# Kernel optimization log

Measured on AMD Instinct MI355X. Metric: run time of the kernel, lower is better.

## Reference

```python
import jax, jax.numpy as jnp
import numpy as np
import math

HEAD = 4
HEAD_DIM = 16
K_ATT = 7
PAD_ATT = 3  # (dilation*(kernel_att-1)+1)//2 with dilation=1, kernel_att=7
K_CONV = 3


def closest_factor_to_sqrt(n):
    if n <= 1:
        return n
    sqrt_n = int(math.sqrt(n))
    if sqrt_n * sqrt_n == n:
        return sqrt_n
    best, best_diff = 1, float('inf')
    for i in range(sqrt_n, 0, -1):
        if n % i == 0:
            diff = abs(i - n // i)
            if diff < best_diff:
                best_diff, best = diff, i
    return best


def setup_inputs() -> dict:
    key = jax.random.key(0)
    ks = jax.random.split(key, 10)
    Cin, Cout = 64, 64
    x = jax.random.normal(ks[0], (2, Cin, 8, 32, 32), dtype=jnp.float32)
    w1 = jax.random.normal(ks[1], (Cout, Cin), dtype=jnp.float32) * 0.05
    b1 = jax.random.normal(ks[2], (Cout,), dtype=jnp.float32) * 0.01
    w2 = jax.random.normal(ks[3], (Cout, Cin), dtype=jnp.float32) * 0.05
    b2 = jax.random.normal(ks[4], (Cout,), dtype=jnp.float32) * 0.01
    w3 = jax.random.normal(ks[5], (Cout, Cin), dtype=jnp.float32) * 0.05
    b3 = jax.random.normal(ks[6], (Cout,), dtype=jnp.float32) * 0.01
    wp = jax.random.normal(ks[7], (HEAD_DIM, 3), dtype=jnp.float32) * 0.05
    bp = jnp.zeros((HEAD_DIM,), dtype=jnp.float32)
    wfc = jax.random.normal(ks[8], (K_CONV * K_CONV, 3 * HEAD), dtype=jnp.float32) * 0.05
    # dep_conv init per reset_parameters(): identity shift kernels, zero bias
    ident = jnp.eye(K_CONV * K_CONV, dtype=jnp.float32).reshape(K_CONV * K_CONV, K_CONV, K_CONV)
    wdep = jnp.tile(ident[None], (Cout, 1, 1, 1))  # (Cout, 9, 3, 3), groups=head_dim
    bdep = jnp.zeros((Cout,), dtype=jnp.float32)
    rate1 = jnp.array(0.5, dtype=jnp.float32)
    rate2 = jnp.array(0.5, dtype=jnp.float32)
    return {'x': x, 'w1': w1, 'b1': b1, 'w2': w2, 'b2': b2, 'w3': w3, 'b3': b3,
            'wp': wp, 'bp': bp, 'wfc': wfc, 'wdep': wdep, 'bdep': bdep,
            'rate1': rate1, 'rate2': rate2}


def _forward(x, w1, b1, w2, b2, w3, b3, wp, bp, wfc, wdep, bdep, rate1, rate2):
    conv1x1 = lambda t, wm, bias: jnp.einsum('oc,bcdwh->bodwh', wm, t) + bias[None, :, None, None, None]
    q = conv1x1(x, w1, b1)
    k = conv1x1(x, w2, b2)
    v = conv1x1(x, w3, b3)
    b, C, d, w, h = q.shape
    scaling = HEAD_DIM ** -0.5
    fh = closest_factor_to_sqrt(d)
    fw = d // fh
    H2, W2 = fh * h, fw * w  # flat reshape of (d, w, h) -> (H2, W2)

    # position encoding, torch position(d, h, w) -> (1, 3, d, w, h)
    loc_d = jnp.broadcast_to(jnp.linspace(-1.0, 1.0, d)[:, None, None], (d, w, h))
    loc_w = jnp.broadcast_to(jnp.linspace(-1.0, 1.0, w)[None, :, None], (d, w, h))
    loc_h = jnp.broadcast_to(jnp.linspace(-1.0, 1.0, h)[None, None, :], (d, w, h))
    loc = jnp.stack([loc_d, loc_w, loc_h], 0)[None].astype(x.dtype)
    pe = (jnp.einsum('oc,bcdwh->bodwh', wp, loc) + bp[None, :, None, None, None])
    pe = pe.reshape(1, HEAD_DIM, H2, W2)

    q_att = (q * scaling).reshape(b * HEAD, HEAD_DIM, H2, W2)
    k_att = k.reshape(b * HEAD, HEAD_DIM, H2, W2)
    v_att = v.reshape(b * HEAD, HEAD_DIM, H2, W2)

    def unfold(t):
        # nn.Unfold(kernel=7, stride=1) after ReflectionPad2d(3): (N, C, 49, H2, W2)
        p = jnp.pad(t, ((0, 0), (0, 0), (PAD_ATT, PAD_ATT), (PAD_ATT, PAD_ATT)), mode='reflect')
        return jnp.stack([p[:, :, i:i + H2, j:j + W2]
                          for i in range(K_ATT) for j in range(K_ATT)], axis=2)

    unfold_k = unfold(k_att)            # (b*head, hd, 49, H2, W2)
    unfold_rpe = unfold(pe)             # (1, hd, 49, H2, W2)
    scores = unfold_k + pe[:, :, None] - unfold_rpe
    att = jnp.einsum('nchw,nckhw->nkhw', q_att, scores)  # sum over head_dim
    att = jax.nn.softmax(att, axis=1)   # softmax over 49 window positions
    out_att = jnp.einsum('nkhw,nckhw->nchw', att, unfold(v_att))
    out_att = out_att.reshape(b, C, d, w, h)

    # conv-mixing branch
    L = d * w * h
    qkv = jnp.concatenate([q.reshape(b, HEAD, HEAD_DIM, L),
                           k.reshape(b, HEAD, HEAD_DIM, L),
                           v.reshape(b, HEAD, HEAD_DIM, L)], axis=1)  # (b, 3*head, hd, L)
    # fc: 1x1x1 conv over the 3*head channel axis (torch applies it unbatched after permute)
    f_all = jnp.einsum('oc,bcml->boml', wfc, qkv)         # (b, 9, hd, L)
    f_conv = f_all.reshape(b, K_CONV * K_CONV * HEAD_DIM, d, h * w)
    out_conv = jax.lax.conv_general_dilated(
        f_conv, wdep, window_strides=(1, 1), padding=[(1, 1), (1, 1)],
        dimension_numbers=('NCHW', 'OIHW', 'NCHW'), feature_group_count=HEAD_DIM)
    out_conv = out_conv + bdep[None, :, None, None]
    out_conv = out_conv.reshape(b, C, d, w, h)

    return rate1 * out_att + rate2 * out_conv


def reference(x, w1, b1, w2, b2, w3, b3, wp, bp, wfc, wdep, bdep, rate1, rate2):
    return _forward(x, w1, b1, w2, b2, w3, b3, wp, bp, wfc, wdep, bdep, rate1, rate2)
```

## Files before the change

### kernel.cpp

```cpp
#include <hip/hip_runtime.h>


__global__ __launch_bounds__(512) void qkvf_kernel(
    const float* __restrict__ x,
    const float* __restrict__ w1, const float* __restrict__ b1,
    const float* __restrict__ w2, const float* __restrict__ b2,
    const float* __restrict__ w3, const float* __restrict__ b3,
    const float* __restrict__ wfc,
    float* __restrict__ q, float* __restrict__ k, float* __restrict__ v,
    float* __restrict__ f)
{
    __shared__ float xs[64][64];
    __shared__ float wlds[3][64][64];

    int bx    = blockIdx.x;
    int ltile = bx & 127;
    int b     = bx >> 7;
    int l0    = ltile * 64;

    {
        float4* wl = (float4*)wlds;
        for (int t = threadIdx.x; t < 3072; t += 512) {
            int m   = t >> 10;
            int idx = t & 1023;
            const float* src = (m == 0) ? w1 : (m == 1) ? w2 : w3;
            wl[t] = ((const float4*)src)[idx];
        }
    }
    const float4* xg = (const float4*)(x + (size_t)b * 64 * 8192);
    for (int t = threadIdx.x; t < 1024; t += 512) {
        int ci = t >> 4, col = t & 15;
        *((float4*)&xs[ci][col * 4]) = xg[ci * 2048 + (l0 >> 2) + col];
    }
    __syncthreads();

    int lane = threadIdx.x & 63;
    int wv   = __builtin_amdgcn_readfirstlane(threadIdx.x >> 6);
    int l    = l0 + lane;
    int hd0  = 2 * wv;

    float qa[4][2], ka[4][2], va[4][2];
#pragma unroll
    for (int hh = 0; hh < 4; ++hh)
#pragma unroll
        for (int p = 0; p < 2; ++p) {
            int c = hh * 16 + hd0 + p;
            qa[hh][p] = b1[c]; ka[hh][p] = b2[c]; va[hh][p] = b3[c];
        }

#pragma unroll 4
    for (int c4 = 0; c4 < 16; ++c4) {
        float xv[4];
#pragma unroll
        for (int u = 0; u < 4; ++u) xv[u] = xs[c4 * 4 + u][lane];
#pragma unroll
        for (int hh = 0; hh < 4; ++hh)
#pragma unroll
            for (int p = 0; p < 2; ++p) {
                int c = hh * 16 + hd0 + p;
                float4 wq = *(const float4*)&wlds[0][c][c4 * 4];
                float4 wk = *(const float4*)&wlds[1][c][c4 * 4];
                float4 wx = *(const float4*)&wlds[2][c][c4 * 4];
                qa[hh][p] = fmaf(wq.x, xv[0], qa[hh][p]);
                qa[hh][p] = fmaf(wq.y, xv[1], qa[hh][p]);
                qa[hh][p] = fmaf(wq.z, xv[2], qa[hh][p]);
                qa[hh][p] = fmaf(wq.w, xv[3], qa[hh][p]);
                ka[hh][p] = fmaf(wk.x, xv[0], ka[hh][p]);
                ka[hh][p] = fmaf(wk.y, xv[1], ka[hh][p]);
                ka[hh][p] = fmaf(wk.z, xv[2], ka[hh][p]);
                ka[hh][p] = fmaf(wk.w, xv[3], ka[hh][p]);
                va[hh][p] = fmaf(wx.x, xv[0], va[hh][p]);
                va[hh][p] = fmaf(wx.y, xv[1], va[hh][p]);
                va[hh][p] = fmaf(wx.z, xv[2], va[hh][p]);
                va[hh][p] = fmaf(wx.w, xv[3], va[hh][p]);
            }
    }

#pragma unroll
    for (int hh = 0; hh < 4; ++hh)
#pragma unroll
        for (int p = 0; p < 2; ++p) {
            int c = hh * 16 + hd0 + p;
            size_t o = (size_t)(b * 64 + c) * 8192 + l;
            q[o] = qa[hh][p]; k[o] = ka[hh][p]; v[o] = va[hh][p];
        }

#pragma unroll
    for (int m = 0; m < 9; ++m)
#pragma unroll
        for (int p = 0; p < 2; ++p) {
            float acc = 0.f;
#pragma unroll
            for (int hh = 0; hh < 4; ++hh) {
                acc = fmaf(wfc[m * 12 + 0 + hh], qa[hh][p], acc);
                acc = fmaf(wfc[m * 12 + 4 + hh], ka[hh][p], acc);
                acc = fmaf(wfc[m * 12 + 8 + hh], va[hh][p], acc);
            }
            int hd = hd0 + p;
            f[((size_t)(b * 9 + m) * 16 + hd) * 8192 + l] = acc;
        }
}

__global__ __launch_bounds__(256) void att_kernel(
    const float* __restrict__ q, const float* __restrict__ k,
    const float* __restrict__ v,
    const float* __restrict__ wp, const float* __restrict__ bp,
    const float* __restrict__ rate1p, float* __restrict__ out)
{
    __shared__ float kp[22][22][20];
    __shared__ float vt[22][22][20];

    int bx = blockIdx.x;
    int xt = bx & 7;
    int yt = (bx >> 3) & 3;
    int n  = bx >> 5;
    int head = n & 3;
    int b    = n >> 2;
    int y0 = yt * 16, x0 = xt * 16;

    const int NELEM = 16 * 22 * 22;
    for (int e = threadIdx.x; e < NELEM; e += 256) {
        int tx  = e % 22;
        int rem = e / 22;
        int ty  = rem % 22;
        int c   = rem / 22;
        int sy = y0 + ty - 3; if (sy < 0) sy = -sy; else if (sy >= 64)  sy = 126 - sy;
        int sx = x0 + tx - 3; if (sx < 0) sx = -sx; else if (sx >= 128) sx = 254 - sx;
        int l = sy * 128 + sx;
        size_t o = (size_t)(b * 64 + head * 16 + c) * 8192 + l;
        int dd = l >> 10, r2 = l & 1023, ww = r2 >> 5, hh = r2 & 31;
        float ld = dd * (2.0f / 7.0f)  - 1.0f;
        float lw = ww * (2.0f / 31.0f) - 1.0f;
        float lh = hh * (2.0f / 31.0f) - 1.0f;
        float pe = bp[c];
        pe = fmaf(wp[c * 3 + 0], ld, pe);
        pe = fmaf(wp[c * 3 + 1], lw, pe);
        pe = fmaf(wp[c * 3 + 2], lh, pe);
        kp[ty][tx][c] = k[o] - pe;
        vt[ty][tx][c] = v[o];
    }
    __syncthreads();

    int tx = threadIdx.x & 15, ty = threadIdx.x >> 4;
    int l = (y0 + ty) * 128 + (x0 + tx);

    float qc[16];
#pragma unroll
    for (int c = 0; c < 16; ++c)
        qc[c] = q[(size_t)(b * 64 + head * 16 + c) * 8192 + l] * 0.25f;

    float lg[49];
#pragma unroll
    for (int i = 0; i < 7; ++i)
#pragma unroll
        for (int j = 0; j < 7; ++j) {
            const float4* p = (const float4*)&kp[ty + i][tx + j][0];
            float4 a = p[0], b4 = p[1], c4 = p[2], d4 = p[3];
            float acc =      qc[0]  * a.x;
            acc = fmaf(qc[1],  a.y,  acc); acc = fmaf(qc[2],  a.z,  acc);
            acc = fmaf(qc[3],  a.w,  acc); acc = fmaf(qc[4],  b4.x, acc);
            acc = fmaf(qc[5],  b4.y, acc); acc = fmaf(qc[6],  b4.z, acc);
            acc = fmaf(qc[7],  b4.w, acc); acc = fmaf(qc[8],  c4.x, acc);
            acc = fmaf(qc[9],  c4.y, acc); acc = fmaf(qc[10], c4.z, acc);
            acc = fmaf(qc[11], c4.w, acc); acc = fmaf(qc[12], d4.x, acc);
            acc = fmaf(qc[13], d4.y, acc); acc = fmaf(qc[14], d4.z, acc);
            acc = fmaf(qc[15], d4.w, acc);
            lg[i * 7 + j] = acc;
        }

    float mx = lg[0];
#pragma unroll
    for (int kk = 1; kk < 49; ++kk) mx = fmaxf(mx, lg[kk]);
    float se = 0.f;
#pragma unroll
    for (int kk = 0; kk < 49; ++kk) { lg[kk] = __expf(lg[kk] - mx); se += lg[kk]; }
    float scale = rate1p[0] / se;

    float oc[16];
#pragma unroll
    for (int c = 0; c < 16; ++c) oc[c] = 0.f;
#pragma unroll
    for (int i = 0; i < 7; ++i)
#pragma unroll
        for (int j = 0; j < 7; ++j) {
            float wgt = lg[i * 7 + j];
            const float4* p = (const float4*)&vt[ty + i][tx + j][0];
            float4 a = p[0], b4 = p[1], c4 = p[2], d4 = p[3];
            oc[0]  = fmaf(wgt, a.x,  oc[0]);  oc[1]  = fmaf(wgt, a.y,  oc[1]);
            oc[2]  = fmaf(wgt, a.z,  oc[2]);  oc[3]  = fmaf(wgt, a.w,  oc[3]);
            oc[4]  = fmaf(wgt, b4.x, oc[4]);  oc[5]  = fmaf(wgt, b4.y, oc[5]);
            oc[6]  = fmaf(wgt, b4.z, oc[6]);  oc[7]  = fmaf(wgt, b4.w, oc[7]);
            oc[8]  = fmaf(wgt, c4.x, oc[8]);  oc[9]  = fmaf(wgt, c4.y, oc[9]);
            oc[10] = fmaf(wgt, c4.z, oc[10]); oc[11] = fmaf(wgt, c4.w, oc[11]);
            oc[12] = fmaf(wgt, d4.x, oc[12]); oc[13] = fmaf(wgt, d4.y, oc[13]);
            oc[14] = fmaf(wgt, d4.z, oc[14]); oc[15] = fmaf(wgt, d4.w, oc[15]);
        }

#pragma unroll
    for (int c = 0; c < 16; ++c)
        out[(size_t)(b * 64 + head * 16 + c) * 8192 + l] = oc[c] * scale;
}

__global__ __launch_bounds__(256) void conv_kernel(
    const float* __restrict__ f,
    const float* __restrict__ wdep, const float* __restrict__ bdep,
    const float* __restrict__ rate2p, float* __restrict__ out)
{
    __shared__ float ft[9][8][130];

    int bx = blockIdx.x;
    int xt = bx & 7;
    int g  = (bx >> 3) & 15;
    int b  = bx >> 7;
    int x0 = xt * 128;

    const int NE = 9 * 8 * 130;
    for (int e = threadIdx.x; e < NE; e += 256) {
        int xx  = e % 130;
        int rem = e / 130;
        int y = rem % 8, i = rem / 8;
        int gx = x0 + xx - 1;
        float val = 0.f;
        if (gx >= 0 && gx < 1024) {
            int c144 = g * 9 + i;
            val = f[((size_t)(b * 144 + c144)) * 8192 + y * 1024 + gx];
        }
        ft[i][y][xx] = val;
    }
    __syncthreads();

    int xl = threadIdx.x & 127;
    int op = __builtin_amdgcn_readfirstlane(threadIdx.x >> 7);
    float rate2 = rate2p[0];

    float acc[2][8];
#pragma unroll
    for (int oo = 0; oo < 2; ++oo)
#pragma unroll
        for (int y = 0; y < 8; ++y) acc[oo][y] = 0.f;

    for (int i = 0; i < 9; ++i) {
        float fr[10][3];
#pragma unroll
        for (int dx = 0; dx < 3; ++dx) { fr[0][dx] = 0.f; fr[9][dx] = 0.f; }
#pragma unroll
        for (int y = 0; y < 8; ++y)
#pragma unroll
            for (int dx = 0; dx < 3; ++dx)
                fr[y + 1][dx] = ft[i][y][xl + dx];
#pragma unroll
        for (int oo = 0; oo < 2; ++oo) {
            int o = g * 4 + op * 2 + oo;
#pragma unroll
            for (int ky = 0; ky < 3; ++ky)
#pragma unroll
                for (int kx = 0; kx < 3; ++kx) {
                    float wvv = wdep[((o * 9 + i) * 3 + ky) * 3 + kx];
#pragma unroll
                    for (int y = 0; y < 8; ++y)
                        acc[oo][y] = fmaf(wvv, fr[y + ky][kx], acc[oo][y]);
                }
        }
    }

#pragma unroll
    for (int oo = 0; oo < 2; ++oo) {
        int o = g * 4 + op * 2 + oo;
        float bd = bdep[o];
#pragma unroll
        for (int y = 0; y < 8; ++y) {
            size_t idx = (size_t)(b * 64 + o) * 8192 + y * 1024 + x0 + xl;
            out[idx] = out[idx] + rate2 * (acc[oo][y] + bd);
        }
    }
}

extern "C" void kernel_launch(void* const* d_in, const int* in_sizes, int n_in,
                              void* d_out, int out_size, void* d_ws, size_t ws_size,
                              hipStream_t stream)
{
    (void)in_sizes; (void)n_in; (void)out_size; (void)ws_size;
    const float* x     = (const float*)d_in[0];
    const float* w1    = (const float*)d_in[1];
    const float* b1    = (const float*)d_in[2];
    const float* w2    = (const float*)d_in[3];
    const float* b2    = (const float*)d_in[4];
    const float* w3    = (const float*)d_in[5];
    const float* b3    = (const float*)d_in[6];
    const float* wp    = (const float*)d_in[7];
    const float* bp    = (const float*)d_in[8];
    const float* wfc   = (const float*)d_in[9];
    const float* wdep  = (const float*)d_in[10];
    const float* bdep  = (const float*)d_in[11];
    const float* rate1 = (const float*)d_in[12];
    const float* rate2 = (const float*)d_in[13];
    float* out = (float*)d_out;

    float* wsf = (float*)d_ws;
    float* q = wsf;
    float* k = wsf + 1048576;
    float* v = wsf + 2097152;
    float* f = wsf + 3145728;

    qkvf_kernel<<<256, 512, 0, stream>>>(x, w1, b1, w2, b2, w3, b3, wfc,
                                         q, k, v, f);
    att_kernel <<<256, 256, 0, stream>>>(q, k, v, wp, bp, rate1, out);
    conv_kernel<<<256, 256, 0, stream>>>(f, wdep, bdep, rate2, out);
}
```

Before: 139.5 us.

## Fuse attention and depthwise conv kernels into one launch

Merges the attention kernel and the grouped conv kernel into a single kernel. After the attention pass it reuses the shared memory to stage the f tiles that map onto the same output pixels, then writes the combined result once. This removes a kernel launch and the read-modify-write of the output buffer. The q scaling also moves into the producer kernel. The conv part now loads a halo per block with redundant f reads, and its 16 accumulators raise register pressure.

```diff
diff --git a/kernel.cpp b/kernel.cpp
--- a/kernel.cpp
+++ b/kernel.cpp
@@ -82,7 +82,8 @@
         for (int p = 0; p < 2; ++p) {
             int c = hh * 16 + hd0 + p;
             size_t o = (size_t)(b * 64 + c) * 8192 + l;
-            q[o] = qa[hh][p]; k[o] = ka[hh][p]; v[o] = va[hh][p];
+            q[o] = qa[hh][p] * 0.25f;
+            k[o] = ka[hh][p]; v[o] = va[hh][p];
         }
 
 #pragma unroll
@@ -101,14 +102,17 @@
         }
 }
 
-__global__ __launch_bounds__(256) void att_kernel(
+__global__ __launch_bounds__(256) void fused_kernel(
     const float* __restrict__ q, const float* __restrict__ k,
-    const float* __restrict__ v,
+    const float* __restrict__ v, const float* __restrict__ f,
     const float* __restrict__ wp, const float* __restrict__ bp,
-    const float* __restrict__ rate1p, float* __restrict__ out)
+    const float* __restrict__ wdep, const float* __restrict__ bdep,
+    const float* __restrict__ rate1p, const float* __restrict__ rate2p,
+    float* __restrict__ out)
 {
-    __shared__ float kp[22][22][20];
-    __shared__ float vt[22][22][20];
+    __shared__ float smem[20736];
+    float* kp = smem;
+    float* vt = smem + 9680;
 
     int bx = blockIdx.x;
     int xt = bx & 7;
@@ -136,8 +140,9 @@
         pe = fmaf(wp[c * 3 + 0], ld, pe);
         pe = fmaf(wp[c * 3 + 1], lw, pe);
         pe = fmaf(wp[c * 3 + 2], lh, pe);
-        kp[ty][tx][c] = k[o] - pe;
-        vt[ty][tx][c] = v[o];
+        int li = (ty * 22 + tx) * 20 + c;
+        kp[li] = k[o] - pe;
+        vt[li] = v[o];
     }
     __syncthreads();
 
@@ -147,14 +152,14 @@
     float qc[16];
 #pragma unroll
     for (int c = 0; c < 16; ++c)
-        qc[c] = q[(size_t)(b * 64 + head * 16 + c) * 8192 + l] * 0.25f;
+        qc[c] = q[(size_t)(b * 64 + head * 16 + c) * 8192 + l];
 
     float lg[49];
 #pragma unroll
     for (int i = 0; i < 7; ++i)
 #pragma unroll
         for (int j = 0; j < 7; ++j) {
-            const float4* p = (const float4*)&kp[ty + i][tx + j][0];
+            const float4* p = (const float4*)&kp[((ty + i) * 22 + tx + j) * 20];
             float4 a = p[0], b4 = p[1], c4 = p[2], d4 = p[3];
             float acc =      qc[0]  * a.x;
             acc = fmaf(qc[1],  a.y,  acc); acc = fmaf(qc[2],  a.z,  acc);
@@ -184,7 +189,7 @@
 #pragma unroll
         for (int j = 0; j < 7; ++j) {
             float wgt = lg[i * 7 + j];
-            const float4* p = (const float4*)&vt[ty + i][tx + j][0];
+            const float4* p = (const float4*)&vt[((ty + i) * 22 + tx + j) * 20];
             float4 a = p[0], b4 = p[1], c4 = p[2], d4 = p[3];
             oc[0]  = fmaf(wgt, a.x,  oc[0]);  oc[1]  = fmaf(wgt, a.y,  oc[1]);
             oc[2]  = fmaf(wgt, a.z,  oc[2]);  oc[3]  = fmaf(wgt, a.w,  oc[3]);
@@ -196,82 +201,64 @@
             oc[14] = fmaf(wgt, d4.z, oc[14]); oc[15] = fmaf(wgt, d4.w, oc[15]);
         }
 
-#pragma unroll
-    for (int c = 0; c < 16; ++c)
-        out[(size_t)(b * 64 + head * 16 + c) * 8192 + l] = oc[c] * scale;
-}
-
-__global__ __launch_bounds__(256) void conv_kernel(
-    const float* __restrict__ f,
-    const float* __restrict__ wdep, const float* __restrict__ bdep,
-    const float* __restrict__ rate2p, float* __restrict__ out)
-{
-    __shared__ float ft[9][8][130];
-
-    int bx = blockIdx.x;
-    int xt = bx & 7;
-    int g  = (bx >> 3) & 15;
-    int b  = bx >> 7;
-    int x0 = xt * 128;
-
-    const int NE = 9 * 8 * 130;
-    for (int e = threadIdx.x; e < NE; e += 256) {
-        int xx  = e % 130;
-        int rem = e / 130;
-        int y = rem % 8, i = rem / 8;
-        int gx = x0 + xx - 1;
+    __syncthreads();
+
+    float* fs = smem;
+    const int NF = 36 * 4 * 8 * 18;
+    const float* fb = f + (size_t)(b * 144 + 36 * head) * 8192;
+    int y2base = (y0 >> 3) - 1;
+    for (int e = threadIdx.x; e < NF; e += 256) {
+        int xo  = e % 18;
+        int r   = e / 18;
+        int s   = r & 7;
+        int r2  = r >> 3;
+        int y2r = r2 & 3;
+        int c36 = r2 >> 2;
+        int y2  = y2base + y2r;
+        int x2  = s * 128 + x0 - 1 + xo;
         float val = 0.f;
-        if (gx >= 0 && gx < 1024) {
-            int c144 = g * 9 + i;
-            val = f[((size_t)(b * 144 + c144)) * 8192 + y * 1024 + gx];
-        }
-        ft[i][y][xx] = val;
-    }
-    __syncthreads();
-
-    int xl = threadIdx.x & 127;
-    int op = __builtin_amdgcn_readfirstlane(threadIdx.x >> 7);
+        if (y2 >= 0 && y2 < 8 && x2 >= 0 && x2 < 1024)
+            val = fb[(size_t)c36 * 8192 + y2 * 1024 + x2];
+        fs[e] = val;
+    }
+    __syncthreads();
+
+    int s    = ty & 7;
+    int y2rp = 1 + (ty >> 3);
+    int xop  = tx + 1;
+
+    float cacc[16];
+#pragma unroll
+    for (int cc = 0; cc < 16; ++cc) cacc[cc] = 0.f;
+
+#pragma unroll 1
+    for (int i = 0; i < 9; ++i) {
+#pragma unroll
+        for (int ky = 0; ky < 3; ++ky)
+#pragma unroll
+            for (int kx = 0; kx < 3; ++kx) {
+                float fv[4];
+#pragma unroll
+                for (int grp = 0; grp < 4; ++grp) {
+                    int c36 = grp * 9 + i;
+                    fv[grp] = fs[((c36 * 4 + y2rp + ky - 1) * 8 + s) * 18
+                                 + xop + kx - 1];
+                }
+#pragma unroll
+                for (int cc = 0; cc < 16; ++cc) {
+                    int o = head * 16 + cc;
+                    float wv = wdep[((o * 9 + i) * 3 + ky) * 3 + kx];
+                    cacc[cc] = fmaf(wv, fv[cc >> 2], cacc[cc]);
+                }
+            }
+    }
+
     float rate2 = rate2p[0];
-
-    float acc[2][8];
-#pragma unroll
-    for (int oo = 0; oo < 2; ++oo)
-#pragma unroll
-        for (int y = 0; y < 8; ++y) acc[oo][y] = 0.f;
-
-    for (int i = 0; i < 9; ++i) {
-        float fr[10][3];
-#pragma unroll
-        for (int dx = 0; dx < 3; ++dx) { fr[0][dx] = 0.f; fr[9][dx] = 0.f; }
-#pragma unroll
-        for (int y = 0; y < 8; ++y)
-#pragma unroll
-            for (int dx = 0; dx < 3; ++dx)
-                fr[y + 1][dx] = ft[i][y][xl + dx];
-#pragma unroll
-        for (int oo = 0; oo < 2; ++oo) {
-            int o = g * 4 + op * 2 + oo;
-#pragma unroll
-            for (int ky = 0; ky < 3; ++ky)
-#pragma unroll
-                for (int kx = 0; kx < 3; ++kx) {
-                    float wvv = wdep[((o * 9 + i) * 3 + ky) * 3 + kx];
-#pragma unroll
-                    for (int y = 0; y < 8; ++y)
-                        acc[oo][y] = fmaf(wvv, fr[y + ky][kx], acc[oo][y]);
-                }
-        }
-    }
-
-#pragma unroll
-    for (int oo = 0; oo < 2; ++oo) {
-        int o = g * 4 + op * 2 + oo;
-        float bd = bdep[o];
-#pragma unroll
-        for (int y = 0; y < 8; ++y) {
-            size_t idx = (size_t)(b * 64 + o) * 8192 + y * 1024 + x0 + xl;
-            out[idx] = out[idx] + rate2 * (acc[oo][y] + bd);
-        }
+#pragma unroll
+    for (int cc = 0; cc < 16; ++cc) {
+        float bd = bdep[head * 16 + cc];
+        out[(size_t)(b * 64 + head * 16 + cc) * 8192 + l]
+            = oc[cc] * scale + rate2 * (cacc[cc] + bd);
     }
 }
 
@@ -302,8 +289,8 @@
     float* v = wsf + 2097152;
     float* f = wsf + 3145728;
 
-    qkvf_kernel<<<256, 512, 0, stream>>>(x, w1, b1, w2, b2, w3, b3, wfc,
-                                         q, k, v, f);
-    att_kernel <<<256, 256, 0, stream>>>(q, k, v, wp, bp, rate1, out);
-    conv_kernel<<<256, 256, 0, stream>>>(f, wdep, bdep, rate2, out);
+    qkvf_kernel <<<256, 512, 0, stream>>>(x, w1, b1, w2, b2, w3, b3, wfc,
+                                          q, k, v, f);
+    fused_kernel<<<256, 256, 0, stream>>>(q, k, v, f, wp, bp, wdep, bdep,
+                                          rate1, rate2, out);
 }
```

Result: slower. 187.0 us (+34.0%).

## Split attention channels across thread pairs and halve conv tile width

Applied to the files above, without the earlier changes.

The attention kernel now uses two threads per pixel, each handling 8 of the 16 head channels. Partial logits are combined with a lane shuffle, and the block grows to 512 threads. The conv kernel uses 64-wide tiles with one output channel per thread, doubling the grid to 512 blocks. The q scaling is moved into the qkv kernel. The aim is more parallelism, lower register pressure and better occupancy on a small 256-block grid, at the cost of duplicated softmax work and extra shuffles.

```diff
diff --git a/kernel.cpp b/kernel.cpp
--- a/kernel.cpp
+++ b/kernel.cpp
@@ -82,7 +82,8 @@
         for (int p = 0; p < 2; ++p) {
             int c = hh * 16 + hd0 + p;
             size_t o = (size_t)(b * 64 + c) * 8192 + l;
-            q[o] = qa[hh][p]; k[o] = ka[hh][p]; v[o] = va[hh][p];
+            q[o] = qa[hh][p] * 0.25f;
+            k[o] = ka[hh][p]; v[o] = va[hh][p];
         }
 
 #pragma unroll
@@ -101,14 +102,14 @@
         }
 }
 
-__global__ __launch_bounds__(256) void att_kernel(
+__global__ __launch_bounds__(512, 4) void att_kernel(
     const float* __restrict__ q, const float* __restrict__ k,
     const float* __restrict__ v,
     const float* __restrict__ wp, const float* __restrict__ bp,
     const float* __restrict__ rate1p, float* __restrict__ out)
 {
-    __shared__ float kp[22][22][20];
-    __shared__ float vt[22][22][20];
+    __shared__ float kp[22 * 22 * 20];
+    __shared__ float vt[22 * 22 * 20];
 
     int bx = blockIdx.x;
     int xt = bx & 7;
@@ -119,7 +120,7 @@
     int y0 = yt * 16, x0 = xt * 16;
 
     const int NELEM = 16 * 22 * 22;
-    for (int e = threadIdx.x; e < NELEM; e += 256) {
+    for (int e = threadIdx.x; e < NELEM; e += 512) {
         int tx  = e % 22;
         int rem = e / 22;
         int ty  = rem % 22;
@@ -136,37 +137,41 @@
         pe = fmaf(wp[c * 3 + 0], ld, pe);
         pe = fmaf(wp[c * 3 + 1], lw, pe);
         pe = fmaf(wp[c * 3 + 2], lh, pe);
-        kp[ty][tx][c] = k[o] - pe;
-        vt[ty][tx][c] = v[o];
+        int li = (ty * 22 + tx) * 20 + c;
+        kp[li] = k[o] - pe;
+        vt[li] = v[o];
     }
     __syncthreads();
 
-    int tx = threadIdx.x & 15, ty = threadIdx.x >> 4;
+    int pix  = threadIdx.x >> 1;
+    int part = threadIdx.x & 1;
+    int tx = pix & 15, ty = pix >> 4;
     int l = (y0 + ty) * 128 + (x0 + tx);
-
-    float qc[16];
-#pragma unroll
-    for (int c = 0; c < 16; ++c)
-        qc[c] = q[(size_t)(b * 64 + head * 16 + c) * 8192 + l] * 0.25f;
+    int cb = part * 8;
+
+    float qc[8];
+#pragma unroll
+    for (int c = 0; c < 8; ++c)
+        qc[c] = q[(size_t)(b * 64 + head * 16 + cb + c) * 8192 + l];
 
     float lg[49];
 #pragma unroll
     for (int i = 0; i < 7; ++i)
 #pragma unroll
         for (int j = 0; j < 7; ++j) {
-            const float4* p = (const float4*)&kp[ty + i][tx + j][0];
-            float4 a = p[0], b4 = p[1], c4 = p[2], d4 = p[3];
-            float acc =      qc[0]  * a.x;
-            acc = fmaf(qc[1],  a.y,  acc); acc = fmaf(qc[2],  a.z,  acc);
-            acc = fmaf(qc[3],  a.w,  acc); acc = fmaf(qc[4],  b4.x, acc);
-            acc = fmaf(qc[5],  b4.y, acc); acc = fmaf(qc[6],  b4.z, acc);
-            acc = fmaf(qc[7],  b4.w, acc); acc = fmaf(qc[8],  c4.x, acc);
-            acc = fmaf(qc[9],  c4.y, acc); acc = fmaf(qc[10], c4.z, acc);
-            acc = fmaf(qc[11], c4.w, acc); acc = fmaf(qc[12], d4.x, acc);
-            acc = fmaf(qc[13], d4.y, acc); acc = fmaf(qc[14], d4.z, acc);
-            acc = fmaf(qc[15], d4.w, acc);
+            const float4* p =
+                (const float4*)&kp[((ty + i) * 22 + tx + j) * 20 + cb];
+            float4 a = p[0], b4 = p[1];
+            float acc =      qc[0] * a.x;
+            acc = fmaf(qc[1], a.y,  acc); acc = fmaf(qc[2], a.z,  acc);
+            acc = fmaf(qc[3], a.w,  acc); acc = fmaf(qc[4], b4.x, acc);
+            acc = fmaf(qc[5], b4.y, acc); acc = fmaf(qc[6], b4.z, acc);
+            acc = fmaf(qc[7], b4.w, acc);
             lg[i * 7 + j] = acc;
         }
+#pragma unroll
+    for (int kk = 0; kk < 49; ++kk)
+        lg[kk] += __shfl_xor(lg[kk], 1, 64);
 
     float mx = lg[0];
 #pragma unroll
@@ -176,29 +181,26 @@
     for (int kk = 0; kk < 49; ++kk) { lg[kk] = __expf(lg[kk] - mx); se += lg[kk]; }
     float scale = rate1p[0] / se;
 
-    float oc[16];
-#pragma unroll
-    for (int c = 0; c < 16; ++c) oc[c] = 0.f;
+    float oc[8];
+#pragma unroll
+    for (int c = 0; c < 8; ++c) oc[c] = 0.f;
 #pragma unroll
     for (int i = 0; i < 7; ++i)
 #pragma unroll
         for (int j = 0; j < 7; ++j) {
             float wgt = lg[i * 7 + j];
-            const float4* p = (const float4*)&vt[ty + i][tx + j][0];
-            float4 a = p[0], b4 = p[1], c4 = p[2], d4 = p[3];
-            oc[0]  = fmaf(wgt, a.x,  oc[0]);  oc[1]  = fmaf(wgt, a.y,  oc[1]);
-            oc[2]  = fmaf(wgt, a.z,  oc[2]);  oc[3]  = fmaf(wgt, a.w,  oc[3]);
-            oc[4]  = fmaf(wgt, b4.x, oc[4]);  oc[5]  = fmaf(wgt, b4.y, oc[5]);
-            oc[6]  = fmaf(wgt, b4.z, oc[6]);  oc[7]  = fmaf(wgt, b4.w, oc[7]);
-            oc[8]  = fmaf(wgt, c4.x, oc[8]);  oc[9]  = fmaf(wgt, c4.y, oc[9]);
-            oc[10] = fmaf(wgt, c4.z, oc[10]); oc[11] = fmaf(wgt, c4.w, oc[11]);
-            oc[12] = fmaf(wgt, d4.x, oc[12]); oc[13] = fmaf(wgt, d4.y, oc[13]);
-            oc[14] = fmaf(wgt, d4.z, oc[14]); oc[15] = fmaf(wgt, d4.w, oc[15]);
-        }
-
-#pragma unroll
-    for (int c = 0; c < 16; ++c)
-        out[(size_t)(b * 64 + head * 16 + c) * 8192 + l] = oc[c] * scale;
+            const float4* p =
+                (const float4*)&vt[((ty + i) * 22 + tx + j) * 20 + cb];
+            float4 a = p[0], b4 = p[1];
+            oc[0] = fmaf(wgt, a.x,  oc[0]); oc[1] = fmaf(wgt, a.y,  oc[1]);
+            oc[2] = fmaf(wgt, a.z,  oc[2]); oc[3] = fmaf(wgt, a.w,  oc[3]);
+            oc[4] = fmaf(wgt, b4.x, oc[4]); oc[5] = fmaf(wgt, b4.y, oc[5]);
+            oc[6] = fmaf(wgt, b4.z, oc[6]); oc[7] = fmaf(wgt, b4.w, oc[7]);
+        }
+
+#pragma unroll
+    for (int c = 0; c < 8; ++c)
+        out[(size_t)(b * 64 + head * 16 + cb + c) * 8192 + l] = oc[c] * scale;
 }
 
 __global__ __launch_bounds__(256) void conv_kernel(
@@ -206,18 +208,18 @@
     const float* __restrict__ wdep, const float* __restrict__ bdep,
     const float* __restrict__ rate2p, float* __restrict__ out)
 {
-    __shared__ float ft[9][8][130];
+    __shared__ float ft[9][8][66];
 
     int bx = blockIdx.x;
-    int xt = bx & 7;
-    int g  = (bx >> 3) & 15;
-    int b  = bx >> 7;
-    int x0 = xt * 128;
-
-    const int NE = 9 * 8 * 130;
+    int xt = bx & 15;
+    int g  = (bx >> 4) & 15;
+    int b  = bx >> 8;
+    int x0 = xt * 64;
+
+    const int NE = 9 * 8 * 66;
     for (int e = threadIdx.x; e < NE; e += 256) {
-        int xx  = e % 130;
-        int rem = e / 130;
+        int xx  = e % 66;
+        int rem = e / 66;
         int y = rem % 8, i = rem / 8;
         int gx = x0 + xx - 1;
         float val = 0.f;
@@ -229,15 +231,14 @@
     }
     __syncthreads();
 
-    int xl = threadIdx.x & 127;
-    int op = __builtin_amdgcn_readfirstlane(threadIdx.x >> 7);
+    int xl = threadIdx.x & 63;
+    int op = __builtin_amdgcn_readfirstlane(threadIdx.x >> 6);
+    int o  = g * 4 + op;
     float rate2 = rate2p[0];
 
-    float acc[2][8];
-#pragma unroll
-    for (int oo = 0; oo < 2; ++oo)
-#pragma unroll
-        for (int y = 0; y < 8; ++y) acc[oo][y] = 0.f;
+    float acc[8];
+#pragma unroll
+    for (int y = 0; y < 8; ++y) acc[y] = 0.f;
 
     for (int i = 0; i < 9; ++i) {
         float fr[10][3];
@@ -249,29 +250,21 @@
             for (int dx = 0; dx < 3; ++dx)
                 fr[y + 1][dx] = ft[i][y][xl + dx];
 #pragma unroll
-        for (int oo = 0; oo < 2; ++oo) {
-            int o = g * 4 + op * 2 + oo;
-#pragma unroll
-            for (int ky = 0; ky < 3; ++ky)
-#pragma unroll
-                for (int kx = 0; kx < 3; ++kx) {
-                    float wvv = wdep[((o * 9 + i) * 3 + ky) * 3 + kx];
-#pragma unroll
-                    for (int y = 0; y < 8; ++y)
-                        acc[oo][y] = fmaf(wvv, fr[y + ky][kx], acc[oo][y]);
-                }
-        }
-    }
-
-#pragma unroll
-    for (int oo = 0; oo < 2; ++oo) {
-        int o = g * 4 + op * 2 + oo;
-        float bd = bdep[o];
-#pragma unroll
-        for (int y = 0; y < 8; ++y) {
-            size_t idx = (size_t)(b * 64 + o) * 8192 + y * 1024 + x0 + xl;
-            out[idx] = out[idx] + rate2 * (acc[oo][y] + bd);
-        }
+        for (int ky = 0; ky < 3; ++ky)
+#pragma unroll
+            for (int kx = 0; kx < 3; ++kx) {
+                float wvv = wdep[((o * 9 + i) * 3 + ky) * 3 + kx];
+#pragma unroll
+                for (int y = 0; y < 8; ++y)
+                    acc[y] = fmaf(wvv, fr[y + ky][kx], acc[y]);
+            }
+    }
+
+    float bd = bdep[o];
+#pragma unroll
+    for (int y = 0; y < 8; ++y) {
+        size_t idx = (size_t)(b * 64 + o) * 8192 + y * 1024 + x0 + xl;
+        out[idx] = out[idx] + rate2 * (acc[y] + bd);
     }
 }
 
@@ -304,6 +297,6 @@
 
     qkvf_kernel<<<256, 512, 0, stream>>>(x, w1, b1, w2, b2, w3, b3, wfc,
                                          q, k, v, f);
-    att_kernel <<<256, 256, 0, stream>>>(q, k, v, wp, bp, rate1, out);
-    conv_kernel<<<256, 256, 0, stream>>>(f, wdep, bdep, rate2, out);
+    att_kernel <<<256, 512, 0, stream>>>(q, k, v, wp, bp, rate1, out);
+    conv_kernel<<<512, 256, 0, stream>>>(f, wdep, bdep, rate2, out);
 }
```

New measurement: 127.1 us. 1.1x faster.
